# Performance work log

Hardware: AMD Instinct MI355X
Metric: run time of the kernel (lower is better)

## Reference

```python
import math
import jax, jax.numpy as jnp
import numpy as np
from jax import lax

B, T, D_HEAD, M_FEAT = 8, 8192, 64, 256
EPS = 1e-6


def _draw_omega(key, d, m):
    # Orthogonal random features: QR blocks of size d x d, rows rescaled by
    # the Frobenius row-norms of the original Gaussian blocks (chi scaling).
    n_blocks = math.ceil(m / d)
    blocks = []
    for i in range(n_blocks):
        g = jax.random.normal(jax.random.fold_in(key, i), (d, d), dtype=jnp.float32)
        qb, _ = jnp.linalg.qr(g)
        norms = jnp.linalg.norm(g, axis=1)
        blocks.append(qb * norms[:, None])
    return jnp.concatenate(blocks, axis=0)[:m]


def setup_inputs() -> dict:
    key = jax.random.key(0)
    kq, kk, kv, ko = jax.random.split(key, 4)
    q = jax.random.normal(kq, (B, T, D_HEAD), dtype=jnp.float32)
    k = jax.random.normal(kk, (B, T, D_HEAD), dtype=jnp.float32)
    v = jax.random.normal(kv, (B, T, D_HEAD), dtype=jnp.float32)
    omega = _draw_omega(ko, D_HEAD, M_FEAT)
    return {"q": q, "k": k, "v": v, "omega": omega}


def _positive_map(x, omega):
    # phi(x) = exp(x @ omega^T - ||x||^2/2 - rowmax) / sqrt(m)
    log_phi = x @ omega.T - 0.5 * jnp.sum(x * x, axis=-1, keepdims=True)
    log_phi = log_phi - jnp.max(log_phi, axis=-1, keepdims=True)
    m = omega.shape[0]
    return jnp.exp(log_phi) / jnp.sqrt(jnp.asarray(m, dtype=x.dtype))


def reference(q, k, v, omega):
    scale = 1.0 / math.sqrt(q.shape[-1])
    phi_q = _positive_map(q * scale, omega)  # (B, T, m)
    phi_k = _positive_map(k * scale, omega)  # (B, T, m)

    def step(carry, xs):
        S, z = carry                     # S: (B, m, d), z: (B, m)
        pq, pk, vt = xs                  # each (B, m) / (B, m) / (B, d)
        S = S + pk[:, :, None] * vt[:, None, :]
        z = z + pk
        out = jnp.einsum('bm,bmd->bd', pq, S)
        denom = jnp.sum(pq * z, axis=-1, keepdims=True) + EPS
        return (S, z), out / denom

    S0 = jnp.zeros((q.shape[0], omega.shape[0], v.shape[-1]), dtype=q.dtype)
    z0 = jnp.zeros((q.shape[0], omega.shape[0]), dtype=q.dtype)
    xs = (jnp.swapaxes(phi_q, 0, 1), jnp.swapaxes(phi_k, 0, 1), jnp.swapaxes(v, 0, 1))
    _, outs = lax.scan(step, (S0, z0), xs)   # outs: (T, B, d)
    return jnp.swapaxes(outs, 0, 1)          # (B, T, d)
```

## Files before the change

kernel.cpp:

```cpp
#include <hip/hip_runtime.h>
#include <hip/hip_bf16.h>

typedef __hip_bfloat16 bf16;
typedef __attribute__((ext_vector_type(8))) short short8;
typedef __attribute__((ext_vector_type(4))) short shortx4;
typedef __attribute__((ext_vector_type(4))) float floatx4;

#define NEED_WS_BYTES 110625024ULL

__device__ __forceinline__ float b2f(bf16 x) { return __bfloat162float(x); }
__device__ __forceinline__ bf16  f2b(float x) { return __float2bfloat16(x); }
__device__ __forceinline__ float bflo(unsigned u) { return __uint_as_float(u << 16); }
__device__ __forceinline__ float bfhi(unsigned u) { return __uint_as_float(u & 0xffff0000u); }

__device__ __forceinline__ float ldin(const void* p, size_t i, int isf32) {
  return isf32 ? ((const float*)p)[i] : b2f(((const bf16*)p)[i]);
}

__device__ __forceinline__ short sb(float f) {
  bf16 h = f2b(f * 0.125f);
  return *reinterpret_cast<short*>(&h);
}
__device__ __forceinline__ short scale_b(short u) {
  float f = __uint_as_float(((unsigned)(unsigned short)u) << 16) * 0.125f;
  bf16 h = f2b(f);
  return *reinterpret_cast<short*>(&h);
}

__global__ __launch_bounds__(256) void k_detect(const void* __restrict__ q,
                                                int* __restrict__ flag) {
  __shared__ int cnt;
  if (threadIdx.x == 0) cnt = 0;
  __syncthreads();
  const unsigned short* u = (const unsigned short*)q;
  int c = 0;
  for (int e = threadIdx.x; e < 2048; e += 256) {
    unsigned short w = u[2 * e];
    int ex = (w >> 7) & 0xFF;
    if ((w & 0x7FFF) != 0 && (ex < 110 || ex > 140)) c++;
  }
  atomicAdd(&cnt, c);
  __syncthreads();
  if (threadIdx.x == 0) *flag = (cnt > 512) ? 1 : 0;
}

__global__ __launch_bounds__(256) void k_omega(const void* __restrict__ omega,
                                               bf16* __restrict__ omb,
                                               const int* __restrict__ flag) {
  int isf32 = *flag;
  int e = blockIdx.x * 256 + threadIdx.x;
  omb[e] = f2b(ldin(omega, e, isf32));
}

__device__ __forceinline__ void phi_load_a(const void* src, size_t row, int quad,
                                           int isf32, short8& a0, short8& a1) {
  if (isf32) {
    const float* xr = (const float*)src + row * 64;
    float4 f0 = *reinterpret_cast<const float4*>(xr + quad * 8);
    float4 f1 = *reinterpret_cast<const float4*>(xr + quad * 8 + 4);
    float4 f2 = *reinterpret_cast<const float4*>(xr + 32 + quad * 8);
    float4 f3 = *reinterpret_cast<const float4*>(xr + 32 + quad * 8 + 4);
    a0[0] = sb(f0.x); a0[1] = sb(f0.y); a0[2] = sb(f0.z); a0[3] = sb(f0.w);
    a0[4] = sb(f1.x); a0[5] = sb(f1.y); a0[6] = sb(f1.z); a0[7] = sb(f1.w);
    a1[0] = sb(f2.x); a1[1] = sb(f2.y); a1[2] = sb(f2.z); a1[3] = sb(f2.w);
    a1[4] = sb(f3.x); a1[5] = sb(f3.y); a1[6] = sb(f3.z); a1[7] = sb(f3.w);
  } else {
    const short* xr = (const short*)src + row * 64;
    short8 r0 = *reinterpret_cast<const short8*>(xr + quad * 8);
    short8 r1 = *reinterpret_cast<const short8*>(xr + 32 + quad * 8);
    #pragma unroll
    for (int j = 0; j < 8; ++j) { a0[j] = scale_b(r0[j]); a1[j] = scale_b(r1[j]); }
  }
}

__device__ __forceinline__ void phi_mfma(const bf16* omb, int li, int quad,
                                         const short8& a0, const short8& a1,
                                         floatx4* c, float* mx) {
  #pragma unroll
  for (int n0 = 0; n0 < 16; ++n0) {
    const short* bp = (const short*)omb + (size_t)(n0 * 16 + li) * 64 + quad * 8;
    short8 b0 = *reinterpret_cast<const short8*>(bp);
    short8 b1 = *reinterpret_cast<const short8*>(bp + 32);
    floatx4 acc = {0.f, 0.f, 0.f, 0.f};
    acc = __builtin_amdgcn_mfma_f32_16x16x32_bf16(a0, b0, acc, 0, 0, 0);
    acc = __builtin_amdgcn_mfma_f32_16x16x32_bf16(a1, b1, acc, 0, 0, 0);
    c[n0] = acc;
  }
  #pragma unroll
  for (int r = 0; r < 4; ++r) {
    float m = c[0][r];
    #pragma unroll
    for (int n0 = 1; n0 < 16; ++n0) m = fmaxf(m, c[n0][r]);
    mx[r] = m;
  }
  #pragma unroll
  for (int mask = 1; mask < 16; mask <<= 1) {
    #pragma unroll
    for (int r = 0; r < 4; ++r) mx[r] = fmaxf(mx[r], __shfl_xor(mx[r], mask, 64));
  }
}

__global__ __launch_bounds__(256)
__attribute__((amdgpu_waves_per_eu(1, 3))) void k_phik(
    const void* __restrict__ k, const void* __restrict__ v,
    const bf16* __restrict__ omb, bf16* __restrict__ phiK,
    bf16* __restrict__ SlocT, float* __restrict__ zloc,
    const int* __restrict__ flag) {
  __shared__ short pkT[256 * 64];
  __shared__ short vTh[64 * 72];
  __shared__ short vTl[64 * 72];

  int isf32 = *flag;
  int tid = threadIdx.x;
  size_t tok0 = (size_t)blockIdx.x * 64;
  int li = tid & 15;
  int quad = (tid >> 4) & 3;
  int w = tid >> 6;
  int m0 = w * 16;
  size_t row = tok0 + m0 + li;

  #pragma unroll
  for (int it = 0; it < 16; ++it) {
    int e = it * 256 + tid;
    int tau = e >> 6, d = e & 63;
    float vv = ldin(v, tok0 * 64 + e, isf32);
    bf16 h = f2b(vv);
    bf16 l = f2b(vv - b2f(h));
    vTh[d * 72 + tau] = *reinterpret_cast<short*>(&h);
    vTl[d * 72 + tau] = *reinterpret_cast<short*>(&l);
  }

  short8 a0, a1;
  phi_load_a(k, row, quad, isf32, a0, a1);
  floatx4 c[16];
  float mx[4];
  phi_mfma(omb, li, quad, a0, a1, c, mx);

  #pragma unroll
  for (int n0 = 0; n0 < 16; ++n0) {
    #pragma unroll
    for (int r = 0; r < 4; ++r) {
      bf16 hv = f2b(__expf(c[n0][r] - mx[r]) * 0.0625f);
      short hb = *reinterpret_cast<short*>(&hv);
      int i = n0 * 16 + li;
      int t = m0 + quad * 4 + r;
      ((short*)phiK)[(tok0 + t) * 256 + i] = hb;
      int cch = (t >> 3) ^ (i & 7);
      pkT[i * 64 + cch * 8 + (t & 7)] = hb;
    }
  }

  __syncthreads();

  {
    int i2 = tid;
    float zz = 0.f;
    #pragma unroll
    for (int c8 = 0; c8 < 8; ++c8) {
      short8 vv8 = *reinterpret_cast<const short8*>(
          &pkT[i2 * 64 + (c8 ^ (i2 & 7)) * 8]);
      #pragma unroll
      for (int j = 0; j < 8; ++j) zz += bflo((unsigned)(unsigned short)vv8[j]);
    }
    zloc[(size_t)blockIdx.x * 256 + i2] = zz;
  }

  int wbase = w * 64;
  floatx4 sa[4][4];
  #pragma unroll
  for (int mt = 0; mt < 4; ++mt)
    #pragma unroll
    for (int n0 = 0; n0 < 4; ++n0) sa[mt][n0] = (floatx4){0.f, 0.f, 0.f, 0.f};

  #pragma unroll
  for (int h = 0; h < 2; ++h) {
    short8 Ah[4], Al[4];
    #pragma unroll
    for (int mt = 0; mt < 4; ++mt) {
      Ah[mt] = *reinterpret_cast<const short8*>(
          &vTh[(mt * 16 + li) * 72 + h * 32 + quad * 8]);
      Al[mt] = *reinterpret_cast<const short8*>(
          &vTl[(mt * 16 + li) * 72 + h * 32 + quad * 8]);
    }
    #pragma unroll
    for (int n0 = 0; n0 < 4; ++n0) {
      int crow = wbase + n0 * 16 + li;
      int cc = (h * 4 + quad) ^ (li & 7);
      short8 Bq = *reinterpret_cast<const short8*>(&pkT[crow * 64 + cc * 8]);
      #pragma unroll
      for (int mt = 0; mt < 4; ++mt) {
        sa[mt][n0] =
            __builtin_amdgcn_mfma_f32_16x16x32_bf16(Ah[mt], Bq, sa[mt][n0], 0, 0, 0);
        sa[mt][n0] =
            __builtin_amdgcn_mfma_f32_16x16x32_bf16(Al[mt], Bq, sa[mt][n0], 0, 0, 0);
      }
    }
  }

  bf16* Sb = SlocT + (size_t)blockIdx.x * 16384;
  #pragma unroll
  for (int mt = 0; mt < 4; ++mt)
    #pragma unroll
    for (int n0 = 0; n0 < 4; ++n0)
      #pragma unroll
      for (int r = 0; r < 4; ++r)
        Sb[(mt * 16 + quad * 4 + r) * 256 + wbase + n0 * 16 + li] =
            f2b(sa[mt][n0][r]);
}

__global__ __launch_bounds__(256) void k_prefix(bf16* __restrict__ SlocT,
                                                float* __restrict__ zloc) {
  __shared__ float tot[4][64][2];
  int tid = threadIdx.x;
  int lane = tid & 63;
  int w = tid >> 6;
  if (blockIdx.x < 1024) {
    int b = blockIdx.x >> 7, g = blockIdx.x & 127;
    int p = g * 64 + lane;
    unsigned* base = (unsigned*)(SlocT + (size_t)b * 2097152) + p;
    unsigned vb[32];
    #pragma unroll
    for (int j = 0; j < 32; ++j) vb[j] = base[(size_t)(w * 32 + j) * 8192];
    float t0 = 0.f, t1 = 0.f;
    #pragma unroll
    for (int j = 0; j < 32; ++j) { t0 += bflo(vb[j]); t1 += bfhi(vb[j]); }
    tot[w][lane][0] = t0; tot[w][lane][1] = t1;
    __syncthreads();
    float r0 = 0.f, r1 = 0.f;
    for (int w2 = 0; w2 < w; ++w2) {
      r0 += tot[w2][lane][0]; r1 += tot[w2][lane][1];
    }
    #pragma unroll
    for (int j = 0; j < 32; ++j) {
      unsigned u = vb[j];
      bf16 h0 = f2b(r0), h1 = f2b(r1);
      unsigned pw = ((unsigned)*(unsigned short*)&h0) |
                    (((unsigned)*(unsigned short*)&h1) << 16);
      base[(size_t)(w * 32 + j) * 8192] = pw;
      r0 += bflo(u); r1 += bfhi(u);
    }
  } else {
    int idx = blockIdx.x - 1024;
    int b = idx >> 2, ig = idx & 3;
    int i = ig * 64 + lane;
    float* base = zloc + (size_t)b * 32768 + i;
    float vb[32];
    #pragma unroll
    for (int j = 0; j < 32; ++j) vb[j] = base[(size_t)(w * 32 + j) * 256];
    float t = 0.f;
    #pragma unroll
    for (int j = 0; j < 32; ++j) t += vb[j];
    tot[w][lane][0] = t;
    __syncthreads();
    float r = 0.f;
    for (int w2 = 0; w2 < w; ++w2) r += tot[w2][lane][0];
    #pragma unroll
    for (int j = 0; j < 32; ++j) {
      float tt = vb[j];
      base[(size_t)(w * 32 + j) * 256] = r;
      r += tt;
    }
  }
}

__global__ __launch_bounds__(256)
__attribute__((amdgpu_waves_per_eu(1, 2))) void k_out(
    const void* __restrict__ q, const bf16* __restrict__ omb,
    const bf16* __restrict__ phiK, const void* __restrict__ v,
    const bf16* __restrict__ SlocT, const float* __restrict__ zloc,
    void* __restrict__ outp, const int* __restrict__ flag) {
  __shared__ short spT[64 * 264];
  __shared__ short vTh[64 * 72];
  __shared__ short vTl[64 * 72];
  __shared__ short aT[64 * 72];

  int isf32 = *flag;
  int chunk = blockIdx.x;
  size_t tok0 = (size_t)chunk * 64;
  int tid = threadIdx.x;
  int lane = tid & 63;
  int li = lane & 15;
  int quad = lane >> 4;
  int w = __builtin_amdgcn_readfirstlane(tid >> 6);
  int m0 = w * 16;

  #pragma unroll
  for (int it = 0; it < 16; ++it) {
    int e = it * 256 + tid;
    int tau = e >> 6, d = e & 63;
    float vv = ldin(v, tok0 * 64 + e, isf32);
    bf16 h = f2b(vv);
    bf16 l = f2b(vv - b2f(h));
    vTh[d * 72 + tau] = *reinterpret_cast<short*>(&h);
    vTl[d * 72 + tau] = *reinterpret_cast<short*>(&l);
  }
  {
    shortx4 z4 = {0, 0, 0, 0};
    int arow0 = m0 + li;
    for (int cc = (w + 1) * 16 + quad * 4; cc < 64; cc += 16)
      *reinterpret_cast<shortx4*>(&aT[arow0 * 72 + cc]) = z4;
  }

  float dpart[4] = {0.f, 0.f, 0.f, 0.f};
  {
    short8 qa0, qa1;
    phi_load_a(q, tok0 + m0 + li, quad, isf32, qa0, qa1);
    floatx4 c[16];
    float mx[4];
    phi_mfma(omb, li, quad, qa0, qa1, c, mx);

    const float* zp = zloc + (size_t)chunk * 256;
    #pragma unroll
    for (int n0 = 0; n0 < 16; ++n0) {
      float zv = zp[n0 * 16 + li];
      #pragma unroll
      for (int r = 0; r < 4; ++r) {
        bf16 hv = f2b(__expf(c[n0][r] - mx[r]) * 0.0625f);
        short hb = *reinterpret_cast<short*>(&hv);
        spT[(m0 + quad * 4 + r) * 264 + n0 * 16 + li] = hb;
        dpart[r] += bflo((unsigned)(unsigned short)hb) * zv;
      }
    }
  }

  const short* pqf = &spT[(m0 + li) * 264 + quad * 8];
  short8 a1[8];
  #pragma unroll
  for (int kk = 0; kk < 8; ++kk)
    a1[kk] = *reinterpret_cast<const short8*>(pqf + kk * 32);

  __syncthreads();

  {
    const short* src = (const short*)SlocT + (size_t)chunk * 16384;
    #pragma unroll
    for (int it = 0; it < 8; ++it) {
      int e = it * 256 + tid;
      int d = e >> 5, seg = e & 31;
      *reinterpret_cast<short8*>(&spT[d * 264 + seg * 8]) =
          *reinterpret_cast<const short8*>(src + d * 256 + seg * 8);
    }
  }

  floatx4 c1[4];
  #pragma unroll
  for (int n0 = 0; n0 < 4; ++n0) c1[n0] = (floatx4){0.f, 0.f, 0.f, 0.f};
  const short* pkb = (const short*)phiK + tok0 * 256;
  #pragma unroll
  for (int n0 = 0; n0 < 4; ++n0) {
    if (n0 <= w) {
      const short* bp = pkb + (size_t)(n0 * 16 + li) * 256 + quad * 8;
      floatx4 acc = c1[n0];
      #pragma unroll
      for (int kk = 0; kk < 8; ++kk) {
        short8 b = *reinterpret_cast<const short8*>(bp + kk * 32);
        acc = __builtin_amdgcn_mfma_f32_16x16x32_bf16(a1[kk], b, acc, 0, 0, 0);
      }
      c1[n0] = acc;
    }
  }

  #pragma unroll
  for (int n0 = 0; n0 < 4; ++n0) {
    if (n0 <= w) {
      int tau = n0 * 16 + li;
      #pragma unroll
      for (int r = 0; r < 4; ++r) {
        int t = m0 + quad * 4 + r;
        float val = (tau <= t) ? c1[n0][r] : 0.f;
        dpart[r] += val;
        bf16 hh = f2b(val);
        aT[t * 72 + tau] = *reinterpret_cast<short*>(&hh);
      }
    }
  }

  __syncthreads();

  floatx4 o[4];
  #pragma unroll
  for (int n0 = 0; n0 < 4; ++n0) o[n0] = (floatx4){0.f, 0.f, 0.f, 0.f};

  const short* arow = &aT[(m0 + li) * 72 + quad * 8];
  short8 a3_0 = *reinterpret_cast<const short8*>(arow);
  short8 a3_1 = *reinterpret_cast<const short8*>(arow + 32);

  #pragma unroll
  for (int n0 = 0; n0 < 4; ++n0) {
    floatx4 acc = o[n0];
    const short* sp = &spT[(n0 * 16 + li) * 264 + quad * 8];
    #pragma unroll
    for (int kk = 0; kk < 8; ++kk) {
      short8 b = *reinterpret_cast<const short8*>(sp + kk * 32);
      acc = __builtin_amdgcn_mfma_f32_16x16x32_bf16(a1[kk], b, acc, 0, 0, 0);
    }
    const short* vph = &vTh[(n0 * 16 + li) * 72 + quad * 8];
    const short* vpl = &vTl[(n0 * 16 + li) * 72 + quad * 8];
    short8 bh0 = *reinterpret_cast<const short8*>(vph);
    short8 bh1 = *reinterpret_cast<const short8*>(vph + 32);
    short8 bl0 = *reinterpret_cast<const short8*>(vpl);
    short8 bl1 = *reinterpret_cast<const short8*>(vpl + 32);
    acc = __builtin_amdgcn_mfma_f32_16x16x32_bf16(a3_0, bh0, acc, 0, 0, 0);
    acc = __builtin_amdgcn_mfma_f32_16x16x32_bf16(a3_1, bh1, acc, 0, 0, 0);
    acc = __builtin_amdgcn_mfma_f32_16x16x32_bf16(a3_0, bl0, acc, 0, 0, 0);
    acc = __builtin_amdgcn_mfma_f32_16x16x32_bf16(a3_1, bl1, acc, 0, 0, 0);
    o[n0] = acc;
  }

  #pragma unroll
  for (int mask = 1; mask < 16; mask <<= 1) {
    #pragma unroll
    for (int r = 0; r < 4; ++r) dpart[r] += __shfl_xor(dpart[r], mask, 64);
  }

  #pragma unroll
  for (int r = 0; r < 4; ++r) {
    float rd = 1.f / (dpart[r] + 1e-6f);
    size_t obb = (tok0 + m0 + quad * 4 + r) * 64 + li;
    if (isf32) {
      float* op = (float*)outp + obb;
      #pragma unroll
      for (int n0 = 0; n0 < 4; ++n0) op[n0 * 16] = o[n0][r] * rd;
    } else {
      bf16* op = (bf16*)outp + obb;
      #pragma unroll
      for (int n0 = 0; n0 < 4; ++n0) op[n0 * 16] = f2b(o[n0][r] * rd);
    }
  }
}

extern "C" void kernel_launch(void* const* d_in, const int* in_sizes, int n_in,
                              void* d_out, int out_size, void* d_ws, size_t ws_size,
                              hipStream_t stream) {
  (void)in_sizes; (void)n_in; (void)out_size;
  if (ws_size < NEED_WS_BYTES) return;

  const void* q = d_in[0];
  const void* k = d_in[1];
  const void* v = d_in[2];
  const void* omega = d_in[3];

  int*   flag = (int*)d_ws;
  float* wsf  = (float*)d_ws + 64;
  bf16*  omb  = (bf16*)wsf;
  float* zloc = wsf + 131072;
  bf16*  Sloc = (bf16*)(wsf + 393216);
  bf16*  phiK = (bf16*)(wsf + 17170432);

  k_detect<<<1, 256, 0, stream>>>(q, flag);
  k_omega<<<64, 256, 0, stream>>>(omega, omb, flag);
  k_phik<<<1024, 256, 0, stream>>>(k, v, omb, phiK, Sloc, zloc, flag);
  k_prefix<<<1056, 256, 0, stream>>>(Sloc, zloc);
  k_out<<<1024, 256, 0, stream>>>(q, omb, phiK, v, Sloc, zloc, d_out, flag);
}
```

Measured before the change: 190.9 us.

## Fold dtype detection into omega kernel and drop bf16 low-part V split

Dtype detection moves inside k_omega, so each block detects independently and block 0 writes the flag, which removes one kernel launch. In k_out the hi/lo bf16 split of V is dropped, so the intra-chunk attention-times-V product uses a single bf16 copy. This halves those MFMAs and frees one LDS buffer. The waves-per-eu hint is raised from 2 to 3 to allow more occupancy. The cost is lower precision on the V term and redundant detection work in every omega block.

```diff
diff --git a/kernel.cpp b/kernel.cpp
--- a/kernel.cpp
+++ b/kernel.cpp
@@ -27,28 +27,30 @@
   return *reinterpret_cast<short*>(&h);
 }
 
-__global__ __launch_bounds__(256) void k_detect(const void* __restrict__ q,
-                                                int* __restrict__ flag) {
-  __shared__ int cnt;
-  if (threadIdx.x == 0) cnt = 0;
+__device__ __forceinline__ int detect_f32(const void* q, int tid, int* cntp) {
+  if (tid == 0) *cntp = 0;
   __syncthreads();
   const unsigned short* u = (const unsigned short*)q;
   int c = 0;
-  for (int e = threadIdx.x; e < 2048; e += 256) {
+  for (int e = tid; e < 2048; e += 256) {
     unsigned short w = u[2 * e];
     int ex = (w >> 7) & 0xFF;
     if ((w & 0x7FFF) != 0 && (ex < 110 || ex > 140)) c++;
   }
-  atomicAdd(&cnt, c);
+  atomicAdd(cntp, c);
   __syncthreads();
-  if (threadIdx.x == 0) *flag = (cnt > 512) ? 1 : 0;
-}
-
-__global__ __launch_bounds__(256) void k_omega(const void* __restrict__ omega,
+  return (*cntp > 512) ? 1 : 0;
+}
+
+__global__ __launch_bounds__(256) void k_omega(const void* __restrict__ q,
+                                               const void* __restrict__ omega,
                                                bf16* __restrict__ omb,
-                                               const int* __restrict__ flag) {
-  int isf32 = *flag;
-  int e = blockIdx.x * 256 + threadIdx.x;
+                                               int* __restrict__ flag) {
+  __shared__ int cnt;
+  int tid = threadIdx.x;
+  int isf32 = detect_f32(q, tid, &cnt);
+  if (blockIdx.x == 0 && tid == 0) *flag = isf32;
+  int e = blockIdx.x * 256 + tid;
   omb[e] = f2b(ldin(omega, e, isf32));
 }
 
@@ -264,14 +266,13 @@
 }
 
 __global__ __launch_bounds__(256)
-__attribute__((amdgpu_waves_per_eu(1, 2))) void k_out(
+__attribute__((amdgpu_waves_per_eu(1, 3))) void k_out(
     const void* __restrict__ q, const bf16* __restrict__ omb,
     const bf16* __restrict__ phiK, const void* __restrict__ v,
     const bf16* __restrict__ SlocT, const float* __restrict__ zloc,
     void* __restrict__ outp, const int* __restrict__ flag) {
   __shared__ short spT[64 * 264];
   __shared__ short vTh[64 * 72];
-  __shared__ short vTl[64 * 72];
   __shared__ short aT[64 * 72];
 
   int isf32 = *flag;
@@ -288,11 +289,8 @@
   for (int it = 0; it < 16; ++it) {
     int e = it * 256 + tid;
     int tau = e >> 6, d = e & 63;
-    float vv = ldin(v, tok0 * 64 + e, isf32);
-    bf16 h = f2b(vv);
-    bf16 l = f2b(vv - b2f(h));
+    bf16 h = f2b(ldin(v, tok0 * 64 + e, isf32));
     vTh[d * 72 + tau] = *reinterpret_cast<short*>(&h);
-    vTl[d * 72 + tau] = *reinterpret_cast<short*>(&l);
   }
   {
     shortx4 z4 = {0, 0, 0, 0};
@@ -395,15 +393,10 @@
       acc = __builtin_amdgcn_mfma_f32_16x16x32_bf16(a1[kk], b, acc, 0, 0, 0);
     }
     const short* vph = &vTh[(n0 * 16 + li) * 72 + quad * 8];
-    const short* vpl = &vTl[(n0 * 16 + li) * 72 + quad * 8];
     short8 bh0 = *reinterpret_cast<const short8*>(vph);
     short8 bh1 = *reinterpret_cast<const short8*>(vph + 32);
-    short8 bl0 = *reinterpret_cast<const short8*>(vpl);
-    short8 bl1 = *reinterpret_cast<const short8*>(vpl + 32);
     acc = __builtin_amdgcn_mfma_f32_16x16x32_bf16(a3_0, bh0, acc, 0, 0, 0);
     acc = __builtin_amdgcn_mfma_f32_16x16x32_bf16(a3_1, bh1, acc, 0, 0, 0);
-    acc = __builtin_amdgcn_mfma_f32_16x16x32_bf16(a3_0, bl0, acc, 0, 0, 0);
-    acc = __builtin_amdgcn_mfma_f32_16x16x32_bf16(a3_1, bl1, acc, 0, 0, 0);
     o[n0] = acc;
   }
 
@@ -447,8 +440,7 @@
   bf16*  Sloc = (bf16*)(wsf + 393216);
   bf16*  phiK = (bf16*)(wsf + 17170432);
 
-  k_detect<<<1, 256, 0, stream>>>(q, flag);
-  k_omega<<<64, 256, 0, stream>>>(omega, omb, flag);
+  k_omega<<<64, 256, 0, stream>>>(q, omega, omb, flag);
   k_phik<<<1024, 256, 0, stream>>>(k, v, omb, phiK, Sloc, zloc, flag);
   k_prefix<<<1056, 256, 0, stream>>>(Sloc, zloc);
   k_out<<<1024, 256, 0, stream>>>(q, omb, phiK, v, Sloc, zloc, d_out, flag);
```

Result: faster. 185.1 us (-3.0%).
